# Optimization experiments

Measured on AMD Instinct MI355X. Metric: run time of the kernel, lower is better.

The kernel has to match this reference:

```python
import jax, jax.numpy as jnp
import numpy as np

B, T, M = 65536, 512, 12  # series, timesteps, seasonal period


def setup_inputs() -> dict:
    key = jax.random.key(0)
    kx, = jax.random.split(key, 1)
    x = jax.random.uniform(kx, (B, T, 1), dtype=jnp.float32) + 0.5  # positive series values
    init_alpha = 0.5 / M
    alpha = jnp.full((1, 1), init_alpha, dtype=jnp.float32)
    beta = jnp.full((1, 1), 0.1 * init_alpha, dtype=jnp.float32)
    phi = jnp.full((1, 1), 0.99, dtype=jnp.float32)
    gamma = jnp.full((1, 1), 0.5, dtype=jnp.float32)
    l0 = jnp.ones((B, 1), dtype=jnp.float32)
    b0 = jnp.zeros((B, 1), dtype=jnp.float32)
    s0 = jnp.ones((B, M), dtype=jnp.float32)
    return {"x": x, "alpha": alpha, "beta": beta, "phi": phi,
            "gamma": gamma, "l0": l0, "b0": b0, "s0": s0}


def reference(x, alpha, beta, phi, gamma, l0, b0, s0):
    # Holt-Winters ESRNN cell: additive trend, multiplicative season, period M.
    # Per step (matching the seasonal+trend branch of the Keras cell):
    #   l = a*(x/s0[:, :1]) + (1-a)*(l0 + b0*phi)
    #   b = be*(l - l0) + (1-be)*(b0*phi)
    #   s_new = g*(x/(l + b*phi)) + (1-g)*s0[:, :1]
    #   s = concat(s0[:,1:], s_new)
    #   out = (l + b*phi) * s0[:, 1:2]
    def step(carry, x_t):
        l_p, b_p, s_p = carry              # (B,1), (B,1), (B,M)
        lb_p = l_p + b_p * phi             # damped trend forecast of level
        l = alpha * (x_t / s_p[:, :1]) + (1.0 - alpha) * lb_p
        b = beta * (l - l_p) + (1.0 - beta) * (b_p * phi)
        s_new = gamma * (x_t / (l + b * phi)) + (1.0 - gamma) * s_p[:, :1]
        s = jnp.concatenate([s_p[:, 1:], s_new], axis=1)
        out = (l + b * phi) * s_p[:, 1:2]
        return (l, b, s), out

    x_tm = jnp.transpose(x, (1, 0, 2))     # (T,B,1) time-major for scan
    _, outs = jax.lax.scan(step, (l0, b0, s0), x_tm)
    return jnp.transpose(outs, (1, 0, 2))  # (B,T,1)
```

## Files before the change

### kernel.cpp

```cpp
#include <hip/hip_runtime.h>


constexpr int TT     = 512;
constexpr int TC     = 96;
constexpr int NCH    = 5;
constexpr int SW     = 64;
constexpr int F4C    = TC / 4;
constexpr int SROW   = 96;
constexpr int PITCH4 = TT / 4;

typedef float f32x4 __attribute__((ext_vector_type(4)));

#define CBAR() asm volatile("" ::: "memory")

#define STEPM(XV, SH, SN, OV)                                              \
    do {                                                                   \
        const float s_h_ = ring[SH];                                       \
        const float q_   = (XV) * __builtin_amdgcn_rcpf(s_h_);             \
        const float lb_  = fmaf(b, phi, l);                                \
        const float ln_  = fmaf(alpha, q_, omal * lb_);                    \
        const float bphi_ = b * phi;                                       \
        const float bn_  = fmaf(beta, ln_ - l, ombe * bphi_);              \
        const float lb2_ = fmaf(bn_, phi, ln_);                            \
        const float sn_  = fmaf(gamma, (XV) * __builtin_amdgcn_rcpf(lb2_), \
                                omg * s_h_);                               \
        (OV) = lb2_ * ring[SN];                                            \
        ring[SH] = sn_;                                                    \
        l = ln_; b = bn_;                                                  \
    } while (0)

__global__ __launch_bounds__(64) void esrnn_kernel(
    const float* __restrict__ x,
    const float* __restrict__ p_alpha,
    const float* __restrict__ p_beta,
    const float* __restrict__ p_phi,
    const float* __restrict__ p_gamma,
    const float* __restrict__ l0,
    const float* __restrict__ b0,
    const float* __restrict__ s0,
    float* __restrict__ out)
{
    const int tid = threadIdx.x;
    const int t7  = tid & 7;
    const int series0 = blockIdx.x * SW;
    const int i = series0 + tid;

    __shared__ __align__(16) float lds[SW * SROW];

    const float alpha = p_alpha[0];
    const float beta  = p_beta[0];
    const float phi   = p_phi[0];
    const float gamma = p_gamma[0];
    const float omal  = 1.0f - alpha;
    const float ombe  = 1.0f - beta;
    const float omg   = 1.0f - gamma;

    float l = l0[i];
    float b = b0[i];

    float ring[12];
    {
        const f32x4* s04 = reinterpret_cast<const f32x4*>(s0 + (size_t)i * 12);
        f32x4 sa = s04[0], sb = s04[1], sc = s04[2];
        ring[0] = sa.x; ring[1] = sa.y; ring[2]  = sa.z; ring[3]  = sa.w;
        ring[4] = sb.x; ring[5] = sb.y; ring[6]  = sb.z; ring[7]  = sb.w;
        ring[8] = sc.x; ring[9] = sc.y; ring[10] = sc.z; ring[11] = sc.w;
    }

    int gx[24], lo[24];
    #pragma unroll
    for (int m = 0; m < 24; ++m) {
        const int f = tid + SW * m;
        const int r = f / 24;
        const int q = f - 24 * r;
        gx[m] = r * PITCH4 + q;
        lo[m] = r * SROW + ((q ^ (r & 7)) << 2);
    }

    const f32x4* x4 = reinterpret_cast<const f32x4*>(x) + (size_t)series0 * PITCH4;
    f32x4*       o4 = reinterpret_cast<f32x4*>(out)     + (size_t)series0 * PITCH4;

    f32x4 vx[24];

    #pragma unroll
    for (int m = 0; m < 24; ++m)
        vx[m] = x4[gx[m]];

    #pragma unroll 1
    for (int k = 0; k < NCH; ++k) {
        #pragma unroll
        for (int m = 0; m < 24; ++m)
            *reinterpret_cast<f32x4*>(&lds[lo[m]]) = vx[m];
        CBAR();

        if (k < NCH - 1) {
            #pragma unroll
            for (int m = 0; m < 24; ++m)
                vx[m] = x4[gx[m] + (k + 1) * F4C];
        } else {
            #pragma unroll
            for (int m = 0; m < 8; ++m) {
                const int f = tid + SW * m;
                vx[m] = x4[(size_t)(f >> 3) * PITCH4 + 120 + (f & 7)];
            }
        }
        CBAR();

        #pragma unroll
        for (int q = 0; q < 24; ++q) {
            const int sl = tid * SROW + ((q ^ t7) << 2);
            const f32x4 xq = *reinterpret_cast<const f32x4*>(&lds[sl]);
            f32x4 oq;
            STEPM(xq.x, (4 * q + 0) % 12, (4 * q + 1) % 12, oq.x);
            STEPM(xq.y, (4 * q + 1) % 12, (4 * q + 2) % 12, oq.y);
            STEPM(xq.z, (4 * q + 2) % 12, (4 * q + 3) % 12, oq.z);
            STEPM(xq.w, (4 * q + 3) % 12, (4 * q + 4) % 12, oq.w);
            *reinterpret_cast<f32x4*>(&lds[sl]) = oq;
        }
        CBAR();

        #pragma unroll
        for (int m = 0; m < 24; ++m) {
            const f32x4 o = *reinterpret_cast<const f32x4*>(&lds[lo[m]]);
            __builtin_nontemporal_store(o, &o4[gx[m] + k * F4C]);
        }
        CBAR();
    }

    {
        #pragma unroll
        for (int m = 0; m < 8; ++m) {
            const int f = tid + SW * m;
            const int rt = f >> 3, qt = f & 7;
            *reinterpret_cast<f32x4*>(&lds[rt * SROW + ((qt ^ (rt & 7)) << 2)]) = vx[m];
        }
        CBAR();
        #pragma unroll
        for (int q = 0; q < 8; ++q) {
            const int sl = tid * SROW + ((q ^ t7) << 2);
            const f32x4 xq = *reinterpret_cast<const f32x4*>(&lds[sl]);
            f32x4 oq;
            STEPM(xq.x, (4 * q + 0) % 12, (4 * q + 1) % 12, oq.x);
            STEPM(xq.y, (4 * q + 1) % 12, (4 * q + 2) % 12, oq.y);
            STEPM(xq.z, (4 * q + 2) % 12, (4 * q + 3) % 12, oq.z);
            STEPM(xq.w, (4 * q + 3) % 12, (4 * q + 4) % 12, oq.w);
            *reinterpret_cast<f32x4*>(&lds[sl]) = oq;
        }
        CBAR();
        #pragma unroll
        for (int m = 0; m < 8; ++m) {
            const int f = tid + SW * m;
            const int rt = f >> 3, qt = f & 7;
            const f32x4 o = *reinterpret_cast<const f32x4*>(
                &lds[rt * SROW + ((qt ^ (rt & 7)) << 2)]);
            __builtin_nontemporal_store(o, &o4[(size_t)rt * PITCH4 + 120 + qt]);
        }
    }
}

extern "C" void kernel_launch(void* const* d_in, const int* in_sizes, int n_in,
                              void* d_out, int out_size, void* d_ws, size_t ws_size,
                              hipStream_t stream)
{
    const float* x       = (const float*)d_in[0];
    const float* p_alpha = (const float*)d_in[1];
    const float* p_beta  = (const float*)d_in[2];
    const float* p_phi   = (const float*)d_in[3];
    const float* p_gamma = (const float*)d_in[4];
    const float* l0      = (const float*)d_in[5];
    const float* b0      = (const float*)d_in[6];
    const float* s0      = (const float*)d_in[7];
    float* out = (float*)d_out;

    const int B = in_sizes[5];
    const int grid = B / SW;

    esrnn_kernel<<<grid, SW, 0, stream>>>(x, p_alpha, p_beta, p_phi, p_gamma,
                                          l0, b0, s0, out);
}
```

Before: 47.82 us.

## Split each series across two blocks, recomputing first half state in second block

Doubles the grid by assigning each 64-series group to two blocks. One block handles the first 256 timesteps, and the other replays the recurrence over the first half without output, then processes the second half. The aim is more waves in flight to hide memory latency of the serial scan. The cost is redundant compute and an extra read of the first half of x. LDS per block also shrinks, and launch bounds request two blocks per CU.

```diff
diff --git a/kernel.cpp b/kernel.cpp
--- a/kernel.cpp
+++ b/kernel.cpp
@@ -1,13 +1,9 @@
 #include <hip/hip_runtime.h>
 
 
-constexpr int TT     = 512;
-constexpr int TC     = 96;
-constexpr int NCH    = 5;
 constexpr int SW     = 64;
-constexpr int F4C    = TC / 4;
-constexpr int SROW   = 96;
-constexpr int PITCH4 = TT / 4;
+constexpr int SROW   = 64;
+constexpr int PITCH4 = 512 / 4;
 
 typedef float f32x4 __attribute__((ext_vector_type(4)));
 
@@ -29,7 +25,101 @@
         l = ln_; b = bn_;                                                  \
     } while (0)
 
-__global__ __launch_bounds__(64) void esrnn_kernel(
+#define STEPC(XV, SH)                                                      \
+    do {                                                                   \
+        const float s_h_ = ring[SH];                                       \
+        const float q_   = (XV) * __builtin_amdgcn_rcpf(s_h_);             \
+        const float lb_  = fmaf(b, phi, l);                                \
+        const float ln_  = fmaf(alpha, q_, omal * lb_);                    \
+        const float bphi_ = b * phi;                                       \
+        const float bn_  = fmaf(beta, ln_ - l, ombe * bphi_);              \
+        const float lb2_ = fmaf(bn_, phi, ln_);                            \
+        const float sn_  = fmaf(gamma, (XV) * __builtin_amdgcn_rcpf(lb2_), \
+                                omg * s_h_);                               \
+        ring[SH] = sn_;                                                    \
+        l = ln_; b = bn_;                                                  \
+    } while (0)
+
+template<int P>
+__device__ __forceinline__ void half_pipeline(
+    const f32x4* __restrict__ x4, f32x4* __restrict__ o4, int base4,
+    int tid, int t7,
+    const int (&gx)[12], const int (&lo)[12],
+    const int (&gxT)[4], const int (&loT)[4],
+    float& l, float& b, float (&ring)[12],
+    float alpha, float beta, float phi, float gamma,
+    float omal, float ombe, float omg,
+    float* lds)
+{
+    f32x4 vx[12], vt[4];
+
+    #pragma unroll
+    for (int m = 0; m < 12; ++m)
+        vx[m] = x4[gx[m] + base4];
+
+    #pragma unroll 1
+    for (int k = 0; k < 5; ++k) {
+        #pragma unroll
+        for (int m = 0; m < 12; ++m)
+            *reinterpret_cast<f32x4*>(&lds[lo[m]]) = vx[m];
+        CBAR();
+
+        if (k < 4) {
+            #pragma unroll
+            for (int m = 0; m < 12; ++m)
+                vx[m] = x4[gx[m] + base4 + (k + 1) * 12];
+        } else {
+            #pragma unroll
+            for (int m = 0; m < 4; ++m)
+                vt[m] = x4[gxT[m] + base4 + 60];
+        }
+        CBAR();
+
+        #pragma unroll
+        for (int q = 0; q < 12; ++q) {
+            const int sl = tid * SROW + ((q ^ t7) << 2);
+            const f32x4 xq = *reinterpret_cast<const f32x4*>(&lds[sl]);
+            f32x4 oq;
+            STEPM(xq.x, (P + 4 * q + 0) % 12, (P + 4 * q + 1) % 12, oq.x);
+            STEPM(xq.y, (P + 4 * q + 1) % 12, (P + 4 * q + 2) % 12, oq.y);
+            STEPM(xq.z, (P + 4 * q + 2) % 12, (P + 4 * q + 3) % 12, oq.z);
+            STEPM(xq.w, (P + 4 * q + 3) % 12, (P + 4 * q + 4) % 12, oq.w);
+            *reinterpret_cast<f32x4*>(&lds[sl]) = oq;
+        }
+        CBAR();
+
+        #pragma unroll
+        for (int m = 0; m < 12; ++m) {
+            const f32x4 o = *reinterpret_cast<const f32x4*>(&lds[lo[m]]);
+            __builtin_nontemporal_store(o, &o4[gx[m] + base4 + k * 12]);
+        }
+        CBAR();
+    }
+
+    #pragma unroll
+    for (int m = 0; m < 4; ++m)
+        *reinterpret_cast<f32x4*>(&lds[loT[m]]) = vt[m];
+    CBAR();
+    #pragma unroll
+    for (int q = 0; q < 4; ++q) {
+        const int sl = tid * SROW + ((q ^ t7) << 2);
+        const f32x4 xq = *reinterpret_cast<const f32x4*>(&lds[sl]);
+        f32x4 oq;
+        STEPM(xq.x, (P + 4 * q + 0) % 12, (P + 4 * q + 1) % 12, oq.x);
+        STEPM(xq.y, (P + 4 * q + 1) % 12, (P + 4 * q + 2) % 12, oq.y);
+        STEPM(xq.z, (P + 4 * q + 2) % 12, (P + 4 * q + 3) % 12, oq.z);
+        STEPM(xq.w, (P + 4 * q + 3) % 12, (P + 4 * q + 4) % 12, oq.w);
+        *reinterpret_cast<f32x4*>(&lds[sl]) = oq;
+    }
+    CBAR();
+    #pragma unroll
+    for (int m = 0; m < 4; ++m) {
+        const f32x4 o = *reinterpret_cast<const f32x4*>(&lds[loT[m]]);
+        __builtin_nontemporal_store(o, &o4[gxT[m] + base4 + 60]);
+    }
+}
+
+__global__ __launch_bounds__(64, 2) void esrnn_kernel(
     const float* __restrict__ x,
     const float* __restrict__ p_alpha,
     const float* __restrict__ p_beta,
@@ -42,7 +132,10 @@
 {
     const int tid = threadIdx.x;
     const int t7  = tid & 7;
-    const int series0 = blockIdx.x * SW;
+    const int g   = blockIdx.x;
+    const int pair = g >> 1;
+    const int h    = g & 1;
+    const int series0 = pair * SW;
     const int i = series0 + tid;
 
     __shared__ __align__(16) float lds[SW * SROW];
@@ -67,94 +160,65 @@
         ring[8] = sc.x; ring[9] = sc.y; ring[10] = sc.z; ring[11] = sc.w;
     }
 
-    int gx[24], lo[24];
-    #pragma unroll
-    for (int m = 0; m < 24; ++m) {
+    int gx[12], lo[12];
+    #pragma unroll
+    for (int m = 0; m < 12; ++m) {
         const int f = tid + SW * m;
-        const int r = f / 24;
-        const int q = f - 24 * r;
+        const int r = f / 12;
+        const int q = f - 12 * r;
         gx[m] = r * PITCH4 + q;
         lo[m] = r * SROW + ((q ^ (r & 7)) << 2);
     }
+    int gxT[4], loT[4];
+    #pragma unroll
+    for (int m = 0; m < 4; ++m) {
+        const int f = tid + SW * m;
+        const int r = f >> 2;
+        const int q = f & 3;
+        gxT[m] = r * PITCH4 + q;
+        loT[m] = r * SROW + ((q ^ (r & 7)) << 2);
+    }
 
     const f32x4* x4 = reinterpret_cast<const f32x4*>(x) + (size_t)series0 * PITCH4;
     f32x4*       o4 = reinterpret_cast<f32x4*>(out)     + (size_t)series0 * PITCH4;
 
-    f32x4 vx[24];
-
-    #pragma unroll
-    for (int m = 0; m < 24; ++m)
-        vx[m] = x4[gx[m]];
-
-    #pragma unroll 1
-    for (int k = 0; k < NCH; ++k) {
-        #pragma unroll
-        for (int m = 0; m < 24; ++m)
-            *reinterpret_cast<f32x4*>(&lds[lo[m]]) = vx[m];
-        CBAR();
-
-        if (k < NCH - 1) {
-            #pragma unroll
-            for (int m = 0; m < 24; ++m)
-                vx[m] = x4[gx[m] + (k + 1) * F4C];
-        } else {
-            #pragma unroll
-            for (int m = 0; m < 8; ++m) {
-                const int f = tid + SW * m;
-                vx[m] = x4[(size_t)(f >> 3) * PITCH4 + 120 + (f & 7)];
+    if (h == 0) {
+        half_pipeline<0>(x4, o4, 0, tid, t7, gx, lo, gxT, loT,
+                         l, b, ring, alpha, beta, phi, gamma,
+                         omal, ombe, omg, lds);
+    } else {
+        const f32x4* xr = reinterpret_cast<const f32x4*>(x) + (size_t)i * PITCH4;
+
+        #pragma unroll 1
+        for (int cg = 0; cg < 5; ++cg) {
+            f32x4 va[12];
+            #pragma unroll
+            for (int j = 0; j < 12; ++j)
+                va[j] = xr[cg * 12 + j];
+            #pragma unroll
+            for (int j = 0; j < 12; ++j) {
+                STEPC(va[j].x, (4 * j + 0) % 12);
+                STEPC(va[j].y, (4 * j + 1) % 12);
+                STEPC(va[j].z, (4 * j + 2) % 12);
+                STEPC(va[j].w, (4 * j + 3) % 12);
             }
         }
-        CBAR();
-
-        #pragma unroll
-        for (int q = 0; q < 24; ++q) {
-            const int sl = tid * SROW + ((q ^ t7) << 2);
-            const f32x4 xq = *reinterpret_cast<const f32x4*>(&lds[sl]);
-            f32x4 oq;
-            STEPM(xq.x, (4 * q + 0) % 12, (4 * q + 1) % 12, oq.x);
-            STEPM(xq.y, (4 * q + 1) % 12, (4 * q + 2) % 12, oq.y);
-            STEPM(xq.z, (4 * q + 2) % 12, (4 * q + 3) % 12, oq.z);
-            STEPM(xq.w, (4 * q + 3) % 12, (4 * q + 4) % 12, oq.w);
-            *reinterpret_cast<f32x4*>(&lds[sl]) = oq;
-        }
-        CBAR();
-
-        #pragma unroll
-        for (int m = 0; m < 24; ++m) {
-            const f32x4 o = *reinterpret_cast<const f32x4*>(&lds[lo[m]]);
-            __builtin_nontemporal_store(o, &o4[gx[m] + k * F4C]);
-        }
-        CBAR();
-    }
-
-    {
-        #pragma unroll
-        for (int m = 0; m < 8; ++m) {
-            const int f = tid + SW * m;
-            const int rt = f >> 3, qt = f & 7;
-            *reinterpret_cast<f32x4*>(&lds[rt * SROW + ((qt ^ (rt & 7)) << 2)]) = vx[m];
-        }
-        CBAR();
-        #pragma unroll
-        for (int q = 0; q < 8; ++q) {
-            const int sl = tid * SROW + ((q ^ t7) << 2);
-            const f32x4 xq = *reinterpret_cast<const f32x4*>(&lds[sl]);
-            f32x4 oq;
-            STEPM(xq.x, (4 * q + 0) % 12, (4 * q + 1) % 12, oq.x);
-            STEPM(xq.y, (4 * q + 1) % 12, (4 * q + 2) % 12, oq.y);
-            STEPM(xq.z, (4 * q + 2) % 12, (4 * q + 3) % 12, oq.z);
-            STEPM(xq.w, (4 * q + 3) % 12, (4 * q + 4) % 12, oq.w);
-            *reinterpret_cast<f32x4*>(&lds[sl]) = oq;
-        }
-        CBAR();
-        #pragma unroll
-        for (int m = 0; m < 8; ++m) {
-            const int f = tid + SW * m;
-            const int rt = f >> 3, qt = f & 7;
-            const f32x4 o = *reinterpret_cast<const f32x4*>(
-                &lds[rt * SROW + ((qt ^ (rt & 7)) << 2)]);
-            __builtin_nontemporal_store(o, &o4[(size_t)rt * PITCH4 + 120 + qt]);
-        }
+        {
+            f32x4 vt4[4];
+            #pragma unroll
+            for (int j = 0; j < 4; ++j)
+                vt4[j] = xr[60 + j];
+            #pragma unroll
+            for (int j = 0; j < 4; ++j) {
+                STEPC(vt4[j].x, (4 * j + 0) % 12);
+                STEPC(vt4[j].y, (4 * j + 1) % 12);
+                STEPC(vt4[j].z, (4 * j + 2) % 12);
+                STEPC(vt4[j].w, (4 * j + 3) % 12);
+            }
+        }
+        half_pipeline<4>(x4, o4, 64, tid, t7, gx, lo, gxT, loT,
+                         l, b, ring, alpha, beta, phi, gamma,
+                         omal, ombe, omg, lds);
     }
 }
 
@@ -173,7 +237,7 @@
     float* out = (float*)d_out;
 
     const int B = in_sizes[5];
-    const int grid = B / SW;
+    const int grid = (B / SW) * 2;
 
     esrnn_kernel<<<grid, SW, 0, stream>>>(x, p_alpha, p_beta, p_phi, p_gamma,
                                           l0, b0, s0, out);
```

Result: slower. 61.79 us (+29.2%).
